# Kernel optimization log

Measured on AMD Instinct MI355X. Metric: run time of the kernel, lower is better.

## Reference

```python
import jax, jax.numpy as jnp
import numpy as np

# Static config (matches init_kwargs / chosen shapes)
B, H, W, C, NH, WS, SS = 8, 56, 56, 1024, 32, 7, 3
N = WS * WS            # tokens per window = 49
HID = 4 * C            # mlp hidden dim
HEAD = C // NH         # 32
SCALE = HEAD ** -0.5


def _rel_pos_index():
    # Same construction as the torch buffer `relative_position_index`
    coords = np.stack(np.meshgrid(np.arange(WS), np.arange(WS), indexing='ij'))  # (2, WS, WS)
    cf = coords.reshape(2, -1)                                    # (2, N)
    rel = (cf[:, :, None] - cf[:, None, :]).transpose(1, 2, 0)    # (N, N, 2)
    rel = rel.copy()
    rel[:, :, 0] += WS - 1
    rel[:, :, 1] += WS - 1
    rel[:, :, 0] *= 2 * WS - 1
    return jnp.asarray(rel.sum(-1))                               # (N, N) int

RPI = _rel_pos_index()


def _shift_mask():
    # Standard Swin cyclic-shift attention mask (0 / -100) for Hp=H, Wp=W
    img = np.zeros((1, H, W, 1), dtype=np.float32)
    cnt = 0
    for hs in (slice(0, -WS), slice(-WS, -SS), slice(-SS, None)):
        for ws in (slice(0, -WS), slice(-WS, -SS), slice(-SS, None)):
            img[:, hs, ws, :] = cnt
            cnt += 1
    mw = img.reshape(1, H // WS, WS, W // WS, WS, 1).transpose(0, 1, 3, 2, 4, 5).reshape(-1, N)
    diff = mw[:, None, :] - mw[:, :, None]
    return jnp.asarray(np.where(diff != 0, -100.0, 0.0).astype(np.float32))  # (nW, N, N)


def _window_partition(t):
    # (B, H, W, D) -> (B*nW, N, D)
    d = t.shape[-1]
    t = t.reshape(B, H // WS, WS, W // WS, WS, d).transpose(0, 1, 3, 2, 4, 5)
    return t.reshape(-1, N, d)


def _window_reverse(w):
    # (B*nW, N, D) -> (B, H, W, D)
    d = w.shape[-1]
    w = w.reshape(B, H // WS, W // WS, WS, WS, d).transpose(0, 1, 3, 2, 4, 5)
    return w.reshape(B, H, W, d)


def _layernorm(t, g, b, eps=1e-5):
    mu = t.mean(-1, keepdims=True)
    var = ((t - mu) ** 2).mean(-1, keepdims=True)
    return (t - mu) * jax.lax.rsqrt(var + eps) * g + b


def setup_inputs() -> dict:
    key = jax.random.key(0)
    ks = jax.random.split(key, 16)
    s = 0.02
    return {
        'x': jax.random.normal(ks[0], (B, H * W, C), jnp.float32),
        'v': jax.random.normal(ks[1], (B, H, W, C), jnp.float32),
        'mask_matrix': _shift_mask(),
        'norm1_g': jnp.ones((C,), jnp.float32),
        'norm1_b': jnp.zeros((C,), jnp.float32),
        'qk_w': jax.random.normal(ks[2], (2 * C, C), jnp.float32) * s,
        'qk_b': jnp.zeros((2 * C,), jnp.float32),
        'rpb_table': jax.random.normal(ks[3], ((2 * WS - 1) ** 2, NH), jnp.float32) * s,
        'proj_w': jax.random.normal(ks[4], (C, C), jnp.float32) * s,
        'proj_b': jnp.zeros((C,), jnp.float32),
        'norm2_g': jnp.ones((C,), jnp.float32),
        'norm2_b': jnp.zeros((C,), jnp.float32),
        'fc1_w': jax.random.normal(ks[5], (HID, C), jnp.float32) * s,
        'fc1_b': jnp.zeros((HID,), jnp.float32),
        'fc2_w': jax.random.normal(ks[6], (C, HID), jnp.float32) * s,
        'fc2_b': jnp.zeros((C,), jnp.float32),
    }


def reference(x, v, mask_matrix, norm1_g, norm1_b, qk_w, qk_b, rpb_table,
              proj_w, proj_b, norm2_g, norm2_b, fc1_w, fc1_b, fc2_w, fc2_b):
    shortcut = x                                             # (B, L, C)
    xn = _layernorm(x, norm1_g, norm1_b).reshape(B, H, W, C)
    # H, W divisible by WS -> no padding. Cyclic shift (shift_size > 0).
    sx = jnp.roll(xn, (-SS, -SS), axis=(1, 2))
    sv = jnp.roll(v, (-SS, -SS), axis=(1, 2))
    xw = _window_partition(sx)                               # (B_, N, C)
    vw = _window_partition(sv)                               # (B_, N, C)
    B_ = xw.shape[0]
    # q, k projections
    qk = (xw @ qk_w.T + qk_b).reshape(B_, N, 2, NH, HEAD)
    q = qk[:, :, 0].transpose(0, 2, 1, 3) * SCALE            # (B_, h, N, d)
    k = qk[:, :, 1].transpose(0, 2, 1, 3)
    attn = jnp.einsum('bhnd,bhmd->bhnm', q, k)               # (B_, h, N, N)
    bias = rpb_table[RPI].transpose(2, 0, 1)                 # (h, N, N)
    attn = attn + bias[None]
    nW = mask_matrix.shape[0]
    attn = attn.reshape(B_ // nW, nW, NH, N, N) + mask_matrix[None, :, None]
    attn = jax.nn.softmax(attn.reshape(B_, NH, N, N), axis=-1)
    vh = vw.reshape(B_, N, NH, HEAD).transpose(0, 2, 1, 3)   # (B_, h, N, d)
    o = jnp.einsum('bhnm,bhmd->bhnd', attn, vh)
    o = o.transpose(0, 2, 1, 3).reshape(B_, N, C)
    o = o @ proj_w.T + proj_b
    # reverse windows and shift
    xr = _window_reverse(o)
    xr = jnp.roll(xr, (SS, SS), axis=(1, 2)).reshape(B, H * W, C)
    x = shortcut + xr                                        # residual (drop_path = 0)
    hdn = _layernorm(x, norm2_g, norm2_b)
    hdn = jax.nn.gelu(hdn @ fc1_w.T + fc1_b, approximate=False)
    hdn = hdn @ fc2_w.T + fc2_b
    return x + hdn
```

## Files before the change

kernel.cpp:

```cpp
#include <hip/hip_runtime.h>
#include <math.h>

typedef __attribute__((ext_vector_type(8))) short bf16x8;
typedef __attribute__((ext_vector_type(4))) short short4v;
typedef __attribute__((ext_vector_type(4))) float f32x4;

#define SCALE 0.17677669529663687f

__device__ __forceinline__ short f2bf(float f) {
  unsigned u = __builtin_bit_cast(unsigned, f);
  unsigned r = u + 0x7fffu + ((u >> 16) & 1u);
  return (short)(r >> 16);
}

__device__ __forceinline__ void gll16(const short* g, short* l) {
  __builtin_amdgcn_global_load_lds(
      (const __attribute__((address_space(1))) unsigned int*)g,
      (__attribute__((address_space(3))) unsigned int*)l, 16, 0, 0);
}

__global__ __launch_bounds__(256) void cast_qkw_kernel(const float* __restrict__ src,
                                                       short* __restrict__ dst) {
  size_t i = (size_t)blockIdx.x * 256 + threadIdx.x;
  f32x4 v = *(const f32x4*)(src + i * 4);
  float sc = (i * 4 < (size_t)1024 * 1024) ? SCALE : 1.0f;
  short4v o;
#pragma unroll
  for (int j = 0; j < 4; ++j) o[j] = f2bf(v[j] * sc);
  *(short4v*)(dst + i * 4) = o;
}

__global__ __launch_bounds__(256) void cast_kernel(const float* __restrict__ src,
                                                   short* __restrict__ dst) {
  size_t i = (size_t)blockIdx.x * 256 + threadIdx.x;
  f32x4 v = *(const f32x4*)(src + i * 4);
  short4v o;
#pragma unroll
  for (int j = 0; j < 4; ++j) o[j] = f2bf(v[j]);
  *(short4v*)(dst + i * 4) = o;
}

__global__ __launch_bounds__(256) void ln1_permute_kernel(
    const float* __restrict__ x,
    const float* __restrict__ g1, const float* __restrict__ b1,
    short* __restrict__ xnw) {
  int r = blockIdx.x;
  int b = r / 3136, rem = r % 3136;
  int wi = rem / 49, n = rem % 49;
  int hs = (wi >> 3) * 7 + n / 7, wsf = (wi & 7) * 7 + n % 7;
  int ho = hs + 3; if (ho >= 56) ho -= 56;
  int wo = wsf + 3; if (wo >= 56) wo -= 56;
  size_t src = ((size_t)b * 3136 + ho * 56 + wo) * 1024;
  int t = threadIdx.x;
  f32x4 xv = *(const f32x4*)(x + src + t * 4);
  float s = xv[0] + xv[1] + xv[2] + xv[3];
  float s2 = xv[0] * xv[0] + xv[1] * xv[1] + xv[2] * xv[2] + xv[3] * xv[3];
#pragma unroll
  for (int m = 1; m < 64; m <<= 1) { s += __shfl_xor(s, m); s2 += __shfl_xor(s2, m); }
  __shared__ float red[8];
  int w = t >> 6;
  if ((t & 63) == 0) { red[w * 2] = s; red[w * 2 + 1] = s2; }
  __syncthreads();
  float ts = red[0] + red[2] + red[4] + red[6];
  float ts2 = red[1] + red[3] + red[5] + red[7];
  float mu = ts * (1.0f / 1024.0f);
  float var = ts2 * (1.0f / 1024.0f) - mu * mu;
  float rs = rsqrtf(var + 1e-5f);
  short4v xo;
#pragma unroll
  for (int j = 0; j < 4; ++j) {
    int cc = t * 4 + j;
    xo[j] = f2bf((xv[j] - mu) * rs * g1[cc] + b1[cc]);
  }
  *(short4v*)(xnw + (size_t)r * 1024 + t * 4) = xo;
}

__global__ __launch_bounds__(256) void ln2_kernel(const float* __restrict__ x2,
                                                  const float* __restrict__ g2,
                                                  const float* __restrict__ b2,
                                                  short* __restrict__ xn2) {
  int r = blockIdx.x;
  size_t src = (size_t)r * 1024;
  int t = threadIdx.x;
  f32x4 xv = *(const f32x4*)(x2 + src + t * 4);
  float s = xv[0] + xv[1] + xv[2] + xv[3];
  float s2 = xv[0] * xv[0] + xv[1] * xv[1] + xv[2] * xv[2] + xv[3] * xv[3];
#pragma unroll
  for (int m = 1; m < 64; m <<= 1) { s += __shfl_xor(s, m); s2 += __shfl_xor(s2, m); }
  __shared__ float red[8];
  int w = t >> 6;
  if ((t & 63) == 0) { red[w * 2] = s; red[w * 2 + 1] = s2; }
  __syncthreads();
  float ts = red[0] + red[2] + red[4] + red[6];
  float ts2 = red[1] + red[3] + red[5] + red[7];
  float mu = ts * (1.0f / 1024.0f);
  float var = ts2 * (1.0f / 1024.0f) - mu * mu;
  float rs = rsqrtf(var + 1e-5f);
  short4v xo;
#pragma unroll
  for (int j = 0; j < 4; ++j) {
    int cc = t * 4 + j;
    xo[j] = f2bf((xv[j] - mu) * rs * g2[cc] + b2[cc]);
  }
  *(short4v*)(xn2 + src + t * 4) = xo;
}

template <int EPI>
__global__ __launch_bounds__(512, 2) void gemm8(const short* __restrict__ A,
                                                const short* __restrict__ Bt,
                                                const float* __restrict__ bias,
                                                const float* __restrict__ add0,
                                                void* __restrict__ out, int N, int K) {
  __shared__ __align__(16) short lds[65536];
  char* basec = (char*)lds;
  int t = threadIdx.x;
  int l = t & 63;
  int w = t >> 6;
  int wm = w >> 2, wn = w & 3;
  int g = l >> 4, c = l & 15;
  int nwg = gridDim.x * gridDim.y;
  int orig = blockIdx.y * gridDim.x + blockIdx.x;
  int q = nwg >> 3, rr = nwg & 7, xcd = orig & 7, idx = orig >> 3;
  int swz = (xcd < rr ? xcd * (q + 1) : rr * (q + 1) + (xcd - rr) * q) + idx;
  int bx = swz % gridDim.x, by = swz / gridDim.x;
  const short* Ab = A + (size_t)bx * 256 * K;
  const short* Bb = Bt + (size_t)by * 256 * K;
  int o0 = t * 16, o1 = 8192 + t * 16;
  int ol0 = o0 ^ (((o0 >> 9) & 1) << 5);
  int ol1 = o1 ^ (((o1 >> 9) & 1) << 5);
  size_t off0 = (size_t)(ol0 >> 6) * K + ((ol0 & 63) >> 1);
  size_t off1 = (size_t)(ol1 >> 6) * K + ((ol1 & 63) >> 1);
  int NT = K >> 6;
  int NI = NT >> 1;

  f32x4 acc[8][4] = {};
  bf16x8 af[8], bf2[2];

#define STAGE_KS(db, ks, tt)                                           \
  do {                                                                 \
    size_t kb = (size_t)(tt) * 64 + (ks) * 32;                         \
    short* rA = (short*)(basec + (db) * 65536 + (ks) * 16384);         \
    short* rB = (short*)(basec + (db) * 65536 + 32768 + (ks) * 16384); \
    gll16(Ab + kb + off0, rA + t * 8);                                 \
    gll16(Ab + kb + off1, rA + 4096 + t * 8);                          \
    gll16(Bb + kb + off0, rB + t * 8);                                 \
    gll16(Bb + kb + off1, rB + 4096 + t * 8);                          \
  } while (0)

#define DSR_A(db, ks)                                                   \
  do {                                                                  \
    _Pragma("unroll") for (int m = 0; m < 8; ++m) {                     \
      int rrow = wm * 128 + m * 16 + c;                                 \
      int lin = rrow * 64 + g * 16;                                     \
      int sw = lin ^ (((lin >> 9) & 1) << 5);                           \
      af[m] = *(const bf16x8*)(basec + (db) * 65536 + (ks) * 16384 + sw); \
    }                                                                   \
  } while (0)

#define DSR_B(db, ks, nh)                                               \
  do {                                                                  \
    _Pragma("unroll") for (int n2 = 0; n2 < 2; ++n2) {                  \
      int rB2 = wn * 64 + ((nh) * 2 + n2) * 16 + c;                     \
      int lin = rB2 * 64 + g * 16;                                      \
      int sw = lin ^ (((lin >> 9) & 1) << 5);                           \
      bf2[n2] = *(const bf16x8*)(basec + (db) * 65536 + 32768 + (ks) * 16384 + sw); \
    }                                                                   \
  } while (0)

#define SB __builtin_amdgcn_sched_barrier(0)

#define PHASE(db, ks, nh, DOSTAGE, sdb, sks, stt)                  \
  do {                                                             \
    if ((nh) == 0) DSR_A(db, ks);                                  \
    DSR_B(db, ks, nh);                                             \
    if (DOSTAGE) {                                                 \
      STAGE_KS(sdb, sks, stt);                                     \
      asm volatile("s_waitcnt vmcnt(8)" ::: "memory");             \
    }                                                              \
    SB;                                                            \
    __builtin_amdgcn_s_barrier();                                  \
    SB;                                                            \
    asm volatile("s_waitcnt lgkmcnt(0)" ::: "memory");             \
    SB;                                                            \
    __builtin_amdgcn_s_setprio(1);                                 \
    _Pragma("unroll") for (int m = 0; m < 8; ++m)                  \
      _Pragma("unroll") for (int n2 = 0; n2 < 2; ++n2)             \
        acc[m][(nh) * 2 + n2] = __builtin_amdgcn_mfma_f32_16x16x32_bf16( \
            af[m], bf2[n2], acc[m][(nh) * 2 + n2], 0, 0, 0);       \
    __builtin_amdgcn_s_setprio(0);                                 \
    SB;                                                            \
    __builtin_amdgcn_s_barrier();                                  \
    SB;                                                            \
  } while (0)

  STAGE_KS(0, 0, 0);
  STAGE_KS(0, 1, 0);
  STAGE_KS(1, 0, 1);
  asm volatile("s_waitcnt vmcnt(8)" ::: "memory");
  SB;
  __builtin_amdgcn_s_barrier();
  SB;

  for (int it = 0; it < NI; ++it) {
    int t1 = 2 * it + 1;
    int nt2 = 2 * it + 2; if (nt2 > NT - 1) nt2 = NT - 1;
    int nt3 = 2 * it + 3; if (nt3 > NT - 1) nt3 = NT - 1;
    PHASE(0, 0, 0, 1, 1, 1, t1);
    PHASE(0, 0, 1, 0, 0, 0, 0);
    PHASE(0, 1, 0, 1, 0, 0, nt2);
    PHASE(0, 1, 1, 0, 0, 0, 0);
    PHASE(1, 0, 0, 1, 0, 1, nt2);
    PHASE(1, 0, 1, 0, 0, 0, 0);
    PHASE(1, 1, 0, 1, 1, 0, nt3);
    PHASE(1, 1, 1, 0, 0, 0, 0);
  }
  asm volatile("s_waitcnt vmcnt(0)" ::: "memory");
#undef PHASE
#undef SB
#undef DSR_B
#undef DSR_A
#undef STAGE_KS

  int mb = bx * 256 + wm * 128;
  int nb = by * 256 + wn * 64;
#pragma unroll
  for (int m = 0; m < 8; ++m) {
#pragma unroll
    for (int i = 0; i < 4; ++i) {
      int row = mb + m * 16 + g * 4 + i;
      size_t orow = row;
      if (EPI == 1) {
        int bb = row / 3136, rem = row % 3136;
        int wi = rem / 49, n = rem % 49;
        int hs = (wi >> 3) * 7 + n / 7, wf = (wi & 7) * 7 + n % 7;
        int ho = hs + 3; if (ho >= 56) ho -= 56;
        int wo = wf + 3; if (wo >= 56) wo -= 56;
        orow = (size_t)bb * 3136 + ho * 56 + wo;
      }
#pragma unroll
      for (int nf = 0; nf < 4; ++nf) {
        int col = nb + nf * 16 + c;
        float val = acc[m][nf][i];
        if (EPI == 0) {
          float bv = bias[col] * (col < 1024 ? SCALE : 1.0f);
          ((short*)out)[(size_t)row * N + col] = f2bf(val + bv);
        } else if (EPI == 1) {
          ((float*)out)[orow * 1024 + col] = val + bias[col] + add0[orow * 1024 + col];
        } else if (EPI == 2) {
          float hv = val + bias[col];
          ((short*)out)[(size_t)row * N + col] = f2bf(0.5f * hv * (1.0f + erff(hv * 0.70710678118f)));
        } else {
          float res = add0[(size_t)row * 1024 + col];
          ((float*)out)[(size_t)row * 1024 + col] = val + bias[col] + res;
        }
      }
    }
  }
}

__global__ __launch_bounds__(256) void attn_kernel(const short* __restrict__ qk,
                                                   const float* __restrict__ v,
                                                   const float* __restrict__ rpb,
                                                   short* __restrict__ ao) {
  __shared__ __align__(16) float rpbt[32 * 169];
  __shared__ int cnt[49];
  __shared__ __align__(16) short Vt[4][32 * 72];
  __shared__ __align__(16) short Pl[4][64 * 72];
  int t = threadIdx.x, l = t & 63, w = t >> 6;
  int win = blockIdx.x >> 3;
  int h = (blockIdx.x & 7) * 4 + w;
  for (int e = t; e < 169 * 32; e += 256) {
    int hh = e / 169, idx = e - hh * 169;
    rpbt[e] = rpb[idx * 32 + hh];
  }
  if (t < 49) {
    int wi = win & 63;
    int hs = (wi >> 3) * 7 + t / 7, wsf = (wi & 7) * 7 + t % 7;
    int rh = hs < 49 ? 0 : (hs < 53 ? 1 : 2);
    int rw = wsf < 49 ? 0 : (wsf < 53 ? 1 : 2);
    cnt[t] = rh * 3 + rw;
  }
  if (l < 49) {
    int wi = win & 63, b = win >> 6;
    int hs = (wi >> 3) * 7 + l / 7, wsf = (wi & 7) * 7 + l % 7;
    int ho = hs + 3; if (ho >= 56) ho -= 56;
    int wo = wsf + 3; if (wo >= 56) wo -= 56;
    const float* vp = v + ((size_t)b * 3136 + ho * 56 + wo) * 1024 + h * 32;
#pragma unroll
    for (int d4 = 0; d4 < 8; ++d4) {
      f32x4 vv = *(const f32x4*)(vp + d4 * 4);
#pragma unroll
      for (int j = 0; j < 4; ++j) Vt[w][(d4 * 4 + j) * 72 + l] = f2bf(vv[j]);
    }
  } else {
#pragma unroll
    for (int d = 0; d < 32; ++d) Vt[w][d * 72 + l] = 0;
  }
  __syncthreads();
  int g = l >> 4, c = l & 15;
  bf16x8 qf[4], kf[4];
#pragma unroll
  for (int mt = 0; mt < 4; ++mt) {
    int r = mt * 16 + c; if (r > 48) r = 48;
    qf[mt] = *(const bf16x8*)&qk[((size_t)win * 49 + r) * 2048 + h * 32 + g * 8];
  }
#pragma unroll
  for (int nt = 0; nt < 4; ++nt) {
    int j = nt * 16 + c; if (j > 48) j = 48;
    kf[nt] = *(const bf16x8*)&qk[((size_t)win * 49 + j) * 2048 + 1024 + h * 32 + g * 8];
  }
  f32x4 s[4][4] = {};
#pragma unroll
  for (int mt = 0; mt < 4; ++mt)
#pragma unroll
    for (int nt = 0; nt < 4; ++nt)
      s[mt][nt] = __builtin_amdgcn_mfma_f32_16x16x32_bf16(qf[mt], kf[nt], s[mt][nt], 0, 0, 0);
#pragma unroll
  for (int mt = 0; mt < 4; ++mt)
#pragma unroll
    for (int nt = 0; nt < 4; ++nt)
#pragma unroll
      for (int i = 0; i < 4; ++i) {
        int r = mt * 16 + g * 4 + i;
        int j = nt * 16 + c;
        float val = s[mt][nt][i];
        if (r < 49 && j < 49) {
          int idx = (r / 7 - j / 7 + 6) * 13 + (r % 7 - j % 7 + 6);
          val += rpbt[h * 169 + idx];
          if (cnt[r] != cnt[j]) val -= 100.0f;
        } else {
          val = -1e30f;
        }
        s[mt][nt][i] = val;
      }
#pragma unroll
  for (int mt = 0; mt < 4; ++mt)
#pragma unroll
    for (int i = 0; i < 4; ++i) {
      float mx = s[mt][0][i];
#pragma unroll
      for (int nt = 1; nt < 4; ++nt) mx = fmaxf(mx, s[mt][nt][i]);
#pragma unroll
      for (int m2 = 1; m2 < 16; m2 <<= 1) mx = fmaxf(mx, __shfl_xor(mx, m2));
      float sum = 0.0f;
#pragma unroll
      for (int nt = 0; nt < 4; ++nt) {
        float e = __expf(s[mt][nt][i] - mx);
        s[mt][nt][i] = e;
        sum += e;
      }
#pragma unroll
      for (int m2 = 1; m2 < 16; m2 <<= 1) sum += __shfl_xor(sum, m2);
      float inv = 1.0f / sum;
#pragma unroll
      for (int nt = 0; nt < 4; ++nt) s[mt][nt][i] *= inv;
    }
#pragma unroll
  for (int mt = 0; mt < 4; ++mt)
#pragma unroll
    for (int nt = 0; nt < 4; ++nt)
#pragma unroll
      for (int i = 0; i < 4; ++i) {
        int r = mt * 16 + g * 4 + i, j = nt * 16 + c;
        Pl[w][r * 72 + j] = f2bf(s[mt][nt][i]);
      }
  __syncthreads();
  f32x4 o[4][2] = {};
#pragma unroll
  for (int kk = 0; kk < 2; ++kk) {
    bf16x8 vb[2];
#pragma unroll
    for (int n2 = 0; n2 < 2; ++n2)
      vb[n2] = *(const bf16x8*)&Vt[w][(n2 * 16 + c) * 72 + kk * 32 + g * 8];
#pragma unroll
    for (int mt = 0; mt < 4; ++mt) {
      bf16x8 pa = *(const bf16x8*)&Pl[w][(mt * 16 + c) * 72 + kk * 32 + g * 8];
#pragma unroll
      for (int n2 = 0; n2 < 2; ++n2)
        o[mt][n2] = __builtin_amdgcn_mfma_f32_16x16x32_bf16(pa, vb[n2], o[mt][n2], 0, 0, 0);
    }
  }
#pragma unroll
  for (int mt = 0; mt < 4; ++mt)
#pragma unroll
    for (int n2 = 0; n2 < 2; ++n2)
#pragma unroll
      for (int i = 0; i < 4; ++i) {
        int r = mt * 16 + g * 4 + i;
        if (r < 49) {
          int d = n2 * 16 + c;
          ao[((size_t)win * 49 + r) * 1024 + h * 32 + d] = f2bf(o[mt][n2][i]);
        }
      }
}

extern "C" void kernel_launch(void* const* d_in, const int* in_sizes, int n_in,
                              void* d_out, int out_size, void* d_ws, size_t ws_size,
                              hipStream_t stream) {
  (void)in_sizes; (void)n_in; (void)out_size; (void)ws_size;
  const float* x = (const float*)d_in[0];
  const float* v = (const float*)d_in[1];
  const float* n1g = (const float*)d_in[3];
  const float* n1b = (const float*)d_in[4];
  const float* qkw = (const float*)d_in[5];
  const float* qkb = (const float*)d_in[6];
  const float* rpb = (const float*)d_in[7];
  const float* pjw = (const float*)d_in[8];
  const float* pjb = (const float*)d_in[9];
  const float* n2g = (const float*)d_in[10];
  const float* n2b = (const float*)d_in[11];
  const float* f1w = (const float*)d_in[12];
  const float* f1b = (const float*)d_in[13];
  const float* f2w = (const float*)d_in[14];
  const float* f2b = (const float*)d_in[15];
  char* ws = (char*)d_ws;
  short* w_qk = (short*)(ws + 0);
  short* w_pj = (short*)(ws + 4194304);
  short* w_f1 = (short*)(ws + 6291456);
  short* w_f2 = (short*)(ws + 14680064);
  short* xnw  = (short*)(ws + 23068672);
  short* qkbuf= (short*)(ws + 74448896);
  short* aob  = (short*)(ws + 23068672);
  short* xn2  = (short*)(ws + 23068672);
  short* h1   = (short*)(ws + 74448896);
  float* out = (float*)d_out;

  cast_qkw_kernel<<<2048, 256, 0, stream>>>(qkw, w_qk);
  cast_kernel<<<1024, 256, 0, stream>>>(pjw, w_pj);
  cast_kernel<<<4096, 256, 0, stream>>>(f1w, w_f1);
  cast_kernel<<<4096, 256, 0, stream>>>(f2w, w_f2);
  ln1_permute_kernel<<<25088, 256, 0, stream>>>(x, n1g, n1b, xnw);
  gemm8<0><<<dim3(98, 8), 512, 0, stream>>>(xnw, w_qk, qkb, nullptr, qkbuf, 2048, 1024);
  attn_kernel<<<4096, 256, 0, stream>>>(qkbuf, v, rpb, aob);
  gemm8<1><<<dim3(98, 4), 512, 0, stream>>>(aob, w_pj, pjb, x, out, 1024, 1024);
  ln2_kernel<<<25088, 256, 0, stream>>>(out, n2g, n2b, xn2);
  for (int ch = 0; ch < 2; ++ch) {
    const short* a1 = xn2 + (size_t)ch * 12544 * 1024;
    float* o2 = out + (size_t)ch * 12544 * 1024;
    gemm8<2><<<dim3(49, 16), 512, 0, stream>>>(a1, w_f1, f1b, nullptr, h1, 4096, 1024);
    gemm8<3><<<dim3(49, 4), 512, 0, stream>>>(h1, w_f2, f2b, o2, o2, 1024, 4096);
  }
}
```

Baseline: 1.070 ms.

## Double-buffer LDS fragment registers to overlap ds_reads with MFMA in GEMM

Restructures the GEMM main loop so the A and B fragments for the next phase are read from LDS into a second register set while the current set feeds MFMAs. The explicit lgkmcnt(0) wait before compute is removed and the compiler now inserts the needed waits. This hides LDS read latency behind matrix math, at the cost of extra VGPRs (a second 8-entry A fragment array), which may reduce occupancy or cause spills. The last READ_A in each iteration prefetches tile 0 of the next iteration, which relies on the staging order being correct.

```diff
diff --git a/kernel.cpp b/kernel.cpp
--- a/kernel.cpp
+++ b/kernel.cpp
@@ -134,7 +134,7 @@
   int NI = NT >> 1;
 
   f32x4 acc[8][4] = {};
-  bf16x8 af[8], bf2[2];
+  bf16x8 afA[8], afB[8], bA[2], bB[2];
 
 #define STAGE_KS(db, ks, tt)                                           \
   do {                                                                 \
@@ -147,46 +147,44 @@
     gll16(Bb + kb + off1, rB + 4096 + t * 8);                          \
   } while (0)
 
-#define DSR_A(db, ks)                                                   \
-  do {                                                                  \
-    _Pragma("unroll") for (int m = 0; m < 8; ++m) {                     \
-      int rrow = wm * 128 + m * 16 + c;                                 \
-      int lin = rrow * 64 + g * 16;                                     \
-      int sw = lin ^ (((lin >> 9) & 1) << 5);                           \
-      af[m] = *(const bf16x8*)(basec + (db) * 65536 + (ks) * 16384 + sw); \
-    }                                                                   \
+#define STAGEV(db, ks, tt)                              \
+  do {                                                  \
+    STAGE_KS(db, ks, tt);                               \
+    asm volatile("s_waitcnt vmcnt(8)" ::: "memory");    \
   } while (0)
 
-#define DSR_B(db, ks, nh)                                               \
-  do {                                                                  \
-    _Pragma("unroll") for (int n2 = 0; n2 < 2; ++n2) {                  \
-      int rB2 = wn * 64 + ((nh) * 2 + n2) * 16 + c;                     \
-      int lin = rB2 * 64 + g * 16;                                      \
-      int sw = lin ^ (((lin >> 9) & 1) << 5);                           \
-      bf2[n2] = *(const bf16x8*)(basec + (db) * 65536 + 32768 + (ks) * 16384 + sw); \
-    }                                                                   \
+#define READ_A(SET, db, ks)                                              \
+  do {                                                                   \
+    _Pragma("unroll") for (int m = 0; m < 8; ++m) {                      \
+      int rrow = wm * 128 + m * 16 + c;                                  \
+      int lin = rrow * 64 + g * 16;                                      \
+      int sw = lin ^ (((lin >> 9) & 1) << 5);                            \
+      SET[m] = *(const bf16x8*)(basec + (db) * 65536 + (ks) * 16384 + sw); \
+    }                                                                    \
   } while (0)
 
+#define READ_B(SET, db, ks, nh)                                          \
+  do {                                                                   \
+    _Pragma("unroll") for (int n2 = 0; n2 < 2; ++n2) {                   \
+      int rB2 = wn * 64 + ((nh) * 2 + n2) * 16 + c;                      \
+      int lin = rB2 * 64 + g * 16;                                       \
+      int sw = lin ^ (((lin >> 9) & 1) << 5);                            \
+      SET[n2] = *(const bf16x8*)(basec + (db) * 65536 + 32768 + (ks) * 16384 + sw); \
+    }                                                                    \
+  } while (0)
+
 #define SB __builtin_amdgcn_sched_barrier(0)
 
-#define PHASE(db, ks, nh, DOSTAGE, sdb, sks, stt)                  \
+#define COMPUTE(ASET, BSET, nh)                                    \
   do {                                                             \
-    if ((nh) == 0) DSR_A(db, ks);                                  \
-    DSR_B(db, ks, nh);                                             \
-    if (DOSTAGE) {                                                 \
-      STAGE_KS(sdb, sks, stt);                                     \
-      asm volatile("s_waitcnt vmcnt(8)" ::: "memory");             \
-    }                                                              \
     SB;                                                            \
     __builtin_amdgcn_s_barrier();                                  \
-    SB;                                                            \
-    asm volatile("s_waitcnt lgkmcnt(0)" ::: "memory");             \
     SB;                                                            \
     __builtin_amdgcn_s_setprio(1);                                 \
     _Pragma("unroll") for (int m = 0; m < 8; ++m)                  \
       _Pragma("unroll") for (int n2 = 0; n2 < 2; ++n2)             \
         acc[m][(nh) * 2 + n2] = __builtin_amdgcn_mfma_f32_16x16x32_bf16( \
-            af[m], bf2[n2], acc[m][(nh) * 2 + n2], 0, 0, 0);       \
+            ASET[m], BSET[n2], acc[m][(nh) * 2 + n2], 0, 0, 0);    \
     __builtin_amdgcn_s_setprio(0);                                 \
     SB;                                                            \
     __builtin_amdgcn_s_barrier();                                  \
@@ -200,25 +198,28 @@
   SB;
   __builtin_amdgcn_s_barrier();
   SB;
+  READ_A(afA, 0, 0);
+  READ_B(bA, 0, 0, 0);
 
   for (int it = 0; it < NI; ++it) {
     int t1 = 2 * it + 1;
     int nt2 = 2 * it + 2; if (nt2 > NT - 1) nt2 = NT - 1;
     int nt3 = 2 * it + 3; if (nt3 > NT - 1) nt3 = NT - 1;
-    PHASE(0, 0, 0, 1, 1, 1, t1);
-    PHASE(0, 0, 1, 0, 0, 0, 0);
-    PHASE(0, 1, 0, 1, 0, 0, nt2);
-    PHASE(0, 1, 1, 0, 0, 0, 0);
-    PHASE(1, 0, 0, 1, 0, 1, nt2);
-    PHASE(1, 0, 1, 0, 0, 0, 0);
-    PHASE(1, 1, 0, 1, 1, 0, nt3);
-    PHASE(1, 1, 1, 0, 0, 0, 0);
+    READ_B(bB, 0, 0, 1); STAGEV(1, 1, t1);    COMPUTE(afA, bA, 0);
+    READ_A(afB, 0, 1);   READ_B(bA, 0, 1, 0); COMPUTE(afA, bB, 1);
+    READ_B(bB, 0, 1, 1); STAGEV(0, 0, nt2);   COMPUTE(afB, bA, 0);
+    READ_A(afA, 1, 0);   READ_B(bA, 1, 0, 0); COMPUTE(afB, bB, 1);
+    READ_B(bB, 1, 0, 1); STAGEV(0, 1, nt2);   COMPUTE(afA, bA, 0);
+    READ_A(afB, 1, 1);   READ_B(bA, 1, 1, 0); COMPUTE(afA, bB, 1);
+    READ_B(bB, 1, 1, 1); STAGEV(1, 0, nt3);   COMPUTE(afB, bA, 0);
+    READ_A(afA, 0, 0);   READ_B(bA, 0, 0, 0); COMPUTE(afB, bB, 1);
   }
   asm volatile("s_waitcnt vmcnt(0)" ::: "memory");
-#undef PHASE
+#undef COMPUTE
 #undef SB
-#undef DSR_B
-#undef DSR_A
+#undef READ_B
+#undef READ_A
+#undef STAGEV
 #undef STAGE_KS
 
   int mb = bx * 256 + wm * 128;
```

Measured after the change: 1.118 ms. +4.6%, slower.

## Split A/B prefetch staging and drop trailing barrier per MFMA phase

Applied to the files above, without the earlier changes.

Splits the per-k-slice global-to-LDS prefetch into separate A and B halves issued in different phases, so loads are spread more finely across the eight phases, and uses tighter vmcnt waits. It also removes the second workgroup barrier after each MFMA block, leaving one barrier per phase. The goal is less synchronization stall and smoother memory/compute overlap in the main GEMM loop. In exchange, the correctness of LDS buffer reuse now depends on the new ordering of stages and waits, which raises the risk of read-after-write hazards.

```diff
diff --git a/kernel.cpp b/kernel.cpp
--- a/kernel.cpp
+++ b/kernel.cpp
@@ -136,15 +136,20 @@
   f32x4 acc[8][4] = {};
   bf16x8 af[8], bf2[2];
 
-#define STAGE_KS(db, ks, tt)                                           \
-  do {                                                                 \
-    size_t kb = (size_t)(tt) * 64 + (ks) * 32;                         \
-    short* rA = (short*)(basec + (db) * 65536 + (ks) * 16384);         \
-    short* rB = (short*)(basec + (db) * 65536 + 32768 + (ks) * 16384); \
-    gll16(Ab + kb + off0, rA + t * 8);                                 \
-    gll16(Ab + kb + off1, rA + 4096 + t * 8);                          \
-    gll16(Bb + kb + off0, rB + t * 8);                                 \
-    gll16(Bb + kb + off1, rB + 4096 + t * 8);                          \
+#define STAGE_A(sdb, sks, tt)                                      \
+  do {                                                             \
+    size_t kb = (size_t)(tt) * 64 + (sks) * 32;                    \
+    short* rA = (short*)(basec + (sdb) * 65536 + (sks) * 16384);   \
+    gll16(Ab + kb + off0, rA + t * 8);                             \
+    gll16(Ab + kb + off1, rA + 4096 + t * 8);                      \
+  } while (0)
+
+#define STAGE_B(sdb, sks, tt)                                              \
+  do {                                                                     \
+    size_t kb = (size_t)(tt) * 64 + (sks) * 32;                            \
+    short* rB = (short*)(basec + (sdb) * 65536 + 32768 + (sks) * 16384);   \
+    gll16(Bb + kb + off0, rB + t * 8);                                     \
+    gll16(Bb + kb + off1, rB + 4096 + t * 8);                              \
   } while (0)
 
 #define DSR_A(db, ks)                                                   \
@@ -169,14 +174,13 @@
 
 #define SB __builtin_amdgcn_sched_barrier(0)
 
-#define PHASE(db, ks, nh, DOSTAGE, sdb, sks, stt)                  \
+#define PHASE(db, ks, nh, STA, STB, sdb, sks, stt, DOW)            \
   do {                                                             \
     if ((nh) == 0) DSR_A(db, ks);                                  \
     DSR_B(db, ks, nh);                                             \
-    if (DOSTAGE) {                                                 \
-      STAGE_KS(sdb, sks, stt);                                     \
-      asm volatile("s_waitcnt vmcnt(8)" ::: "memory");             \
-    }                                                              \
+    if (STA) STAGE_A(sdb, sks, stt);                               \
+    if (STB) STAGE_B(sdb, sks, stt);                               \
+    if (DOW) asm volatile("s_waitcnt vmcnt(2)" ::: "memory");      \
     SB;                                                            \
     __builtin_amdgcn_s_barrier();                                  \
     SB;                                                            \
@@ -188,15 +192,14 @@
         acc[m][(nh) * 2 + n2] = __builtin_amdgcn_mfma_f32_16x16x32_bf16( \
             af[m], bf2[n2], acc[m][(nh) * 2 + n2], 0, 0, 0);       \
     __builtin_amdgcn_s_setprio(0);                                 \
-    SB;                                                            \
-    __builtin_amdgcn_s_barrier();                                  \
-    SB;                                                            \
   } while (0)
 
-  STAGE_KS(0, 0, 0);
-  STAGE_KS(0, 1, 0);
-  STAGE_KS(1, 0, 1);
-  asm volatile("s_waitcnt vmcnt(8)" ::: "memory");
+  STAGE_A(0, 0, 0);
+  STAGE_B(0, 0, 0);
+  STAGE_A(0, 1, 0);
+  STAGE_B(0, 1, 0);
+  STAGE_A(1, 0, 1);
+  asm volatile("s_waitcnt vmcnt(6)" ::: "memory");
   SB;
   __builtin_amdgcn_s_barrier();
   SB;
@@ -205,21 +208,22 @@
     int t1 = 2 * it + 1;
     int nt2 = 2 * it + 2; if (nt2 > NT - 1) nt2 = NT - 1;
     int nt3 = 2 * it + 3; if (nt3 > NT - 1) nt3 = NT - 1;
-    PHASE(0, 0, 0, 1, 1, 1, t1);
-    PHASE(0, 0, 1, 0, 0, 0, 0);
-    PHASE(0, 1, 0, 1, 0, 0, nt2);
-    PHASE(0, 1, 1, 0, 0, 0, 0);
-    PHASE(1, 0, 0, 1, 0, 1, nt2);
-    PHASE(1, 0, 1, 0, 0, 0, 0);
-    PHASE(1, 1, 0, 1, 1, 0, nt3);
-    PHASE(1, 1, 1, 0, 0, 0, 0);
+    PHASE(0, 0, 0, 0, 1, 1, 0, t1, 0);
+    PHASE(0, 0, 1, 1, 0, 1, 1, t1, 1);
+    PHASE(0, 1, 0, 0, 1, 1, 1, t1, 0);
+    PHASE(0, 1, 1, 1, 0, 0, 0, nt2, 0);
+    PHASE(1, 0, 0, 0, 1, 0, 0, nt2, 0);
+    PHASE(1, 0, 1, 1, 0, 0, 1, nt2, 1);
+    PHASE(1, 1, 0, 0, 1, 0, 1, nt2, 0);
+    PHASE(1, 1, 1, 1, 0, 1, 0, nt3, 0);
   }
   asm volatile("s_waitcnt vmcnt(0)" ::: "memory");
 #undef PHASE
 #undef SB
 #undef DSR_B
 #undef DSR_A
-#undef STAGE_KS
+#undef STAGE_B
+#undef STAGE_A
 
   int mb = bx * 256 + wm * 128;
   int nb = by * 256 + wn * 64;
```

New measurement: 1.093 ms. 1.02x slower.
